# Kernel tuning notes

Measured on AMD Instinct MI355X. Metric: run time of the kernel, lower is better.

## Reference

```python
import jax, jax.numpy as jnp
import numpy as np

ALPHA = 0.2  # LeakyReLU negative slope
NEG_INF = -9e15


def setup_inputs() -> dict:
    key = jax.random.key(0)
    k1, k2, k3, k4 = jax.random.split(key, 4)
    B, N, F_in, F_out = 8, 2048, 256, 128
    h = jax.random.normal(k1, (B, N, F_in), dtype=jnp.float32)
    adj = jax.random.randint(k2, (B, N, N), 0, 2, dtype=jnp.int32)
    # xavier_uniform with gain=1.414
    def xavier(k, shape, gain=1.414):
        fan_in, fan_out = shape[0], shape[1]
        limit = gain * np.sqrt(6.0 / (fan_in + fan_out))
        return jax.random.uniform(k, shape, jnp.float32, -limit, limit)
    W = xavier(k3, (F_in, F_out))
    a = xavier(k4, (2 * F_out, 1))
    return {"h": h, "adj": adj, "W": W, "a": a}


def reference(h, adj, W, a):
    # h: [B,N,F_in], adj: [B,N,N], W: [F_in,F_out], a: [2*F_out,1]
    Wh = jnp.einsum('bnf,fe->bne', h, W)  # [B,N,E]
    E = Wh.shape[-1]
    a_src, a_dst = a[:E, 0], a[E:, 0]
    # e[b,i,j] = leakyrelu(Wh[b,i].a_src + Wh[b,j].a_dst)  (additive decomposition
    # of a @ concat(Wh_i, Wh_j) -- same math, no [B,N,N,2E] intermediate)
    s_src = Wh @ a_src  # [B,N]
    s_dst = Wh @ a_dst  # [B,N]
    e = jax.nn.leaky_relu(s_src[:, :, None] + s_dst[:, None, :], negative_slope=ALPHA)
    e = jnp.where(adj > 0, e, NEG_INF)
    attention = jax.nn.softmax(e, axis=2)  # [B,N,N]
    # dropout p=0.0 / eval mode -> identity
    h_prime = jnp.einsum('bij,bje->bie', attention, Wh)
    return jax.nn.elu(h_prime)  # concat=True
```

## Files before the change

### kernel.cpp

```cpp
#include <hip/hip_runtime.h>
#include <hip/hip_bf16.h>

#define GAT_ALPHA 0.2f
#define LOG2E 1.4426950408889634f

typedef float f32x4 __attribute__((ext_vector_type(4)));
typedef int   i32x4 __attribute__((ext_vector_type(4)));
typedef short bf16x8 __attribute__((ext_vector_type(8)));

static constexpr int Nn  = 2048;
static constexpr int FIN = 256;
static constexpr int FO  = 128;

static __device__ __forceinline__ unsigned short f2bf(float x) {
    __hip_bfloat16 h = __float2bfloat16(x);
    return __builtin_bit_cast(unsigned short, h);
}
static __device__ __forceinline__ float bf2f(unsigned short u) {
    unsigned int v = ((unsigned int)u) << 16;
    return __builtin_bit_cast(float, v);
}

__global__ __launch_bounds__(256) void gat_prep(
        const float* __restrict__ W, const float* __restrict__ a,
        float* __restrict__ wa, unsigned int* __restrict__ md_key)
{
    __shared__ float pr[32][8];
    __shared__ float pd[32][8];
    const int t = threadIdx.x;
    const int kl = t >> 3, seg = t & 7;
    const int k = blockIdx.x * 32 + kl;
    float ps = 0.f, pv = 0.f;
    const float* wr = W + (size_t)k * FO + seg * 16;
    #pragma unroll
    for (int f = 0; f < 16; f += 4) {
        f32x4 wv = *(const f32x4*)(wr + f);
        f32x4 as = *(const f32x4*)(a + seg * 16 + f);
        f32x4 ad = *(const f32x4*)(a + FO + seg * 16 + f);
        ps += wv[0]*as[0] + wv[1]*as[1] + wv[2]*as[2] + wv[3]*as[3];
        pv += wv[0]*ad[0] + wv[1]*ad[1] + wv[2]*ad[2] + wv[3]*ad[3];
    }
    pr[kl][seg] = ps; pd[kl][seg] = pv;
    __syncthreads();
    if (t < 32) {
        float s = 0.f, d = 0.f;
        #pragma unroll
        for (int j = 0; j < 8; ++j) { s += pr[t][j]; d += pd[t][j]; }
        wa[blockIdx.x * 32 + t]       = s;
        wa[256 + blockIdx.x * 32 + t] = d;
    }
    if (blockIdx.x == 0 && t < 8) md_key[t] = 0u;
}

__global__ __launch_bounds__(256) void gat_wh(
        const float* __restrict__ h, const float* __restrict__ W,
        const float* __restrict__ wa, unsigned short* __restrict__ Wp,
        float* __restrict__ s_src, float* __restrict__ s_dst,
        unsigned int* __restrict__ md_key)
{
    __shared__ unsigned short WT[FO][264];
    __shared__ float wal[512];
    __shared__ float sred[64][4][2];
    __shared__ float red64[64];
    const int t  = threadIdx.x;
    const int b  = blockIdx.x & 7;
    const int n0 = (blockIdx.x >> 3) << 6;

    if (t < 128) *(f32x4*)&wal[t * 4] = *(const f32x4*)&wa[t * 4];
    #pragma unroll
    for (int c = 0; c < 32; ++c) {
        int flat = c * 1024 + t * 4;
        int k = flat >> 7, f = flat & 127;
        f32x4 wv = *(const f32x4*)&W[flat];
        WT[f + 0][k] = f2bf(wv[0]);
        WT[f + 1][k] = f2bf(wv[1]);
        WT[f + 2][k] = f2bf(wv[2]);
        WT[f + 3][k] = f2bf(wv[3]);
    }
    __syncthreads();

    {
        const int row = t >> 2, seg = t & 3;
        const float* hp  = h + ((size_t)(b * Nn + n0 + row)) * FIN + seg * 64;
        const float* was = &wal[seg * 64];
        const float* wad = &wal[256 + seg * 64];
        float ps = 0.f, pv = 0.f;
        #pragma unroll
        for (int j = 0; j < 64; j += 4) {
            f32x4 hv = *(const f32x4*)(hp + j);
            f32x4 sv = *(const f32x4*)(was + j);
            f32x4 dv = *(const f32x4*)(wad + j);
            ps += hv[0]*sv[0] + hv[1]*sv[1] + hv[2]*sv[2] + hv[3]*sv[3];
            pv += hv[0]*dv[0] + hv[1]*dv[1] + hv[2]*dv[2] + hv[3]*dv[3];
        }
        sred[row][seg][0] = ps;
        sred[row][seg][1] = pv;
    }
    __syncthreads();
    if (t < 64) {
        float s = sred[t][0][0] + sred[t][1][0] + sred[t][2][0] + sred[t][3][0];
        float d = sred[t][0][1] + sred[t][1][1] + sred[t][2][1] + sred[t][3][1];
        s_src[b * Nn + n0 + t] = s;
        s_dst[b * Nn + n0 + t] = d;
        red64[t] = d;
    }
    __syncthreads();
    if (t < 16) red64[t] = fmaxf(fmaxf(red64[t], red64[t + 16]),
                                 fmaxf(red64[t + 32], red64[t + 48]));
    __syncthreads();
    if (t == 0) {
        float m = red64[0];
        #pragma unroll
        for (int j = 1; j < 16; ++j) m = fmaxf(m, red64[j]);
        unsigned int bits = __builtin_bit_cast(unsigned int, m);
        unsigned int key  = (bits & 0x80000000u) ? ~bits : (bits | 0x80000000u);
        atomicMax(md_key + b, key);
    }

    const int w = t >> 6, lane = t & 63, n16 = lane & 15, quad = lane >> 4;
    const float* ha = h + ((size_t)(b * Nn + n0 + w * 16 + n16)) * FIN + quad * 8;
    f32x4 acc[8] = {};
    #pragma unroll
    for (int ks = 0; ks < 8; ++ks) {
        f32x4 h0 = *(const f32x4*)(ha + ks * 32);
        f32x4 h1 = *(const f32x4*)(ha + ks * 32 + 4);
        bf16x8 af;
        af[0] = (short)f2bf(h0[0]); af[1] = (short)f2bf(h0[1]);
        af[2] = (short)f2bf(h0[2]); af[3] = (short)f2bf(h0[3]);
        af[4] = (short)f2bf(h1[0]); af[5] = (short)f2bf(h1[1]);
        af[6] = (short)f2bf(h1[2]); af[7] = (short)f2bf(h1[3]);
        #pragma unroll
        for (int nt = 0; nt < 8; ++nt) {
            bf16x8 bfr = *(const bf16x8*)&WT[nt * 16 + n16][ks * 32 + quad * 8];
            acc[nt] = __builtin_amdgcn_mfma_f32_16x16x32_bf16(af, bfr, acc[nt], 0, 0, 0);
        }
    }
    {
        const int v      = (n0 >> 5) + (w >> 1);
        const int quad_p = ((w & 1) << 1) + (quad >> 1);
        const int eoff   = (quad & 1) << 2;
        #pragma unroll
        for (int nt = 0; nt < 8; ++nt) {
            ushort4 pk;
            pk.x = f2bf(acc[nt][0]); pk.y = f2bf(acc[nt][1]);
            pk.z = f2bf(acc[nt][2]); pk.w = f2bf(acc[nt][3]);
            size_t idx = ((((size_t)(b << 6) + v) * 8 + nt) * 64 + quad_p * 16 + n16) * 8 + eoff;
            *(ushort4*)&Wp[idx] = pk;
        }
    }
}

__global__ __launch_bounds__(512, 2) void gat_attn(
        const int* __restrict__ adj, const unsigned short* __restrict__ Wp,
        const float* __restrict__ s_src, const float* __restrict__ s_dst,
        const unsigned int* __restrict__ md_key, float* __restrict__ out)
{
    constexpr int AS = 132;
    constexpr int MS = 68;
    __shared__ __align__(16) float smem_f[2 * 64 * AS];
    __shared__ __align__(16) unsigned int mlds[64 * MS];
    __shared__ __align__(16) float dlds[Nn];
    __shared__ float l_red[64];
    unsigned short* ldsw = (unsigned short*)smem_f;

    const int t = threadIdx.x, w = t >> 6, lane = t & 63;
    const int n16 = lane & 15, quad = lane >> 4;
    const int rg = w & 1, jwin = w >> 1;
    const int b  = blockIdx.x & 7;
    const int i0 = (blockIdx.x >> 3) << 6;

    if (t < 64) l_red[t] = 0.f;

    const int* abase = adj + ((size_t)(b * Nn + i0 + w * 8)) * Nn + lane;
    const unsigned short* wsrc = Wp + ((size_t)b << 18);

    int av[16];
    #pragma unroll
    for (int k = 0; k < 16; ++k)
        av[k] = abase[(size_t)(k >> 1) * Nn + ((k & 1) << 6)];
    f32x4 pg[4];
    #pragma unroll
    for (int p = 0; p < 4; ++p)
        pg[p] = *(const f32x4*)(wsrc + p * 4096 + t * 8);
    *(f32x4*)&dlds[t * 4] = *(const f32x4*)(s_dst + b * Nn + t * 4);

    const unsigned int key = md_key[b];
    const unsigned int mb_ = (key & 0x80000000u) ? (key ^ 0x80000000u) : ~key;
    const float mdb = __builtin_bit_cast(float, mb_);
    const int r0 = i0 + rg * 32 + n16;
    const float ssr0 = s_src[b * Nn + r0];
    const float ssr1 = s_src[b * Nn + r0 + 16];
    const float tm0 = ssr0 + mdb, tm1 = ssr1 + mdb;
    const float mi0 = fmaxf(tm0, GAT_ALPHA * tm0) * LOG2E;
    const float mi1 = fmaxf(tm1, GAT_ALPHA * tm1) * LOG2E;
    const float sL0 = ssr0 * LOG2E, sL1 = ssr1 * LOG2E;
    const int jw = (jwin << 5) + (quad << 3);
    const int mrow0 = (rg * 32 + n16) * MS;
    const int mrow1 = mrow0 + 16 * MS;

    #pragma unroll
    for (int k = 0; k < 16; ++k) {
        unsigned long long m = __ballot(av[k] > 0);
        const int rr = k >> 1, c = k & 1;
        if (lane == 0) mlds[(w * 8 + rr) * MS + (c << 1)]     = (unsigned int)m;
        if (lane == 1) mlds[(w * 8 + rr) * MS + (c << 1) + 1] = (unsigned int)(m >> 32);
    }
    #pragma unroll
    for (int p = 0; p < 4; ++p)
        *(f32x4*)&ldsw[p * 4096 + t * 8] = pg[p];

    f32x4 acc[2][8] = {};
    float ls0 = 0.f, ls1 = 0.f;
    __syncthreads();

    for (int s = 0; s < 16; ++s) {
        const int cur = s & 1, nxt = cur ^ 1;
        const int j0 = s << 7;
        if (s < 15) {
            const int coff = (s + 1) << 7;
            #pragma unroll
            for (int k = 0; k < 16; ++k)
                av[k] = abase[(size_t)(k >> 1) * Nn + coff + ((k & 1) << 6)];
        }
        f32x4 g[4];
        if (s < 15) {
            const unsigned short* src = wsrc + (size_t)(s + 1) * 16384;
            #pragma unroll
            for (int p = 0; p < 4; ++p)
                g[p] = *(const f32x4*)(src + p * 4096 + t * 8);
        }
        const unsigned int mw0 = mlds[mrow0 + (s << 2) + jwin];
        const unsigned int mw1 = mlds[mrow1 + (s << 2) + jwin];
        const unsigned int mb0 = (mw0 >> (quad << 3)) & 0xffu;
        const unsigned int mb1 = (mw1 >> (quad << 3)) & 0xffu;
        f32x4 d0 = *(const f32x4*)&dlds[j0 + jw];
        f32x4 d1 = *(const f32x4*)&dlds[j0 + jw + 4];

        bf16x8 af0, af1;
        #pragma unroll
        for (int j = 0; j < 4; ++j) {
            {   float u  = __builtin_fmaf(d0[j], LOG2E, sL0);
                float lr = fmaxf(u, GAT_ALPHA * u);
                float e  = __builtin_amdgcn_exp2f(lr - mi0);
                e = ((mb0 >> j) & 1u) ? e : 0.f;
                unsigned short us = f2bf(e);
                ls0 += bf2f(us); af0[j] = (short)us; }
            {   float u  = __builtin_fmaf(d1[j], LOG2E, sL0);
                float lr = fmaxf(u, GAT_ALPHA * u);
                float e  = __builtin_amdgcn_exp2f(lr - mi0);
                e = ((mb0 >> (4 + j)) & 1u) ? e : 0.f;
                unsigned short us = f2bf(e);
                ls0 += bf2f(us); af0[4 + j] = (short)us; }
            {   float u  = __builtin_fmaf(d0[j], LOG2E, sL1);
                float lr = fmaxf(u, GAT_ALPHA * u);
                float e  = __builtin_amdgcn_exp2f(lr - mi1);
                e = ((mb1 >> j) & 1u) ? e : 0.f;
                unsigned short us = f2bf(e);
                ls1 += bf2f(us); af1[j] = (short)us; }
            {   float u  = __builtin_fmaf(d1[j], LOG2E, sL1);
                float lr = fmaxf(u, GAT_ALPHA * u);
                float e  = __builtin_amdgcn_exp2f(lr - mi1);
                e = ((mb1 >> (4 + j)) & 1u) ? e : 0.f;
                unsigned short us = f2bf(e);
                ls1 += bf2f(us); af1[4 + j] = (short)us; }
        }

        const unsigned short* bbase = &ldsw[cur * 16384 + (jwin << 12) + (lane << 3)];
        #pragma unroll
        for (int nt = 0; nt < 8; ++nt) {
            bf16x8 bfr = *(const bf16x8*)(bbase + (nt << 9));
            acc[0][nt] = __builtin_amdgcn_mfma_f32_16x16x32_bf16(af0, bfr, acc[0][nt], 0, 0, 0);
            acc[1][nt] = __builtin_amdgcn_mfma_f32_16x16x32_bf16(af1, bfr, acc[1][nt], 0, 0, 0);
        }

        if (s < 15) {
            #pragma unroll
            for (int k = 0; k < 16; ++k) {
                unsigned long long m = __ballot(av[k] > 0);
                const int rr = k >> 1, c = k & 1;
                const int wd = ((s + 1) << 2) + (c << 1);
                if (lane == 0) mlds[(w * 8 + rr) * MS + wd]     = (unsigned int)m;
                if (lane == 1) mlds[(w * 8 + rr) * MS + wd + 1] = (unsigned int)(m >> 32);
            }
            #pragma unroll
            for (int p = 0; p < 4; ++p)
                *(f32x4*)&ldsw[nxt * 16384 + p * 4096 + t * 8] = g[p];
        }
        __syncthreads();
    }

    ls0 += __shfl_xor(ls0, 16); ls0 += __shfl_xor(ls0, 32);
    ls1 += __shfl_xor(ls1, 16); ls1 += __shfl_xor(ls1, 32);
    if (quad == 0) {
        atomicAdd(&l_red[rg * 32 + n16], ls0);
        atomicAdd(&l_red[rg * 32 + 16 + n16], ls1);
    }

    float* slot = smem_f + (size_t)(jwin & 1) * (64 * AS);
    const int rbase = rg * 32;
    if (jwin < 2) {
        #pragma unroll
        for (int ig = 0; ig < 2; ++ig)
            #pragma unroll
            for (int nt = 0; nt < 8; ++nt)
                #pragma unroll
                for (int rr = 0; rr < 4; ++rr)
                    slot[(size_t)(rbase + ig * 16 + quad * 4 + rr) * AS + nt * 16 + n16] = acc[ig][nt][rr];
    }
    __syncthreads();
    if (jwin >= 2) {
        #pragma unroll
        for (int ig = 0; ig < 2; ++ig)
            #pragma unroll
            for (int nt = 0; nt < 8; ++nt)
                #pragma unroll
                for (int rr = 0; rr < 4; ++rr)
                    slot[(size_t)(rbase + ig * 16 + quad * 4 + rr) * AS + nt * 16 + n16] += acc[ig][nt][rr];
    }
    __syncthreads();

    float* ob = out + ((size_t)(b * Nn + i0)) * FO;
    #pragma unroll
    for (int c = 0; c < 4; ++c) {
        int flat = c * 2048 + t * 4;
        int m = flat >> 7, f = flat & 127;
        f32x4 v0 = *(const f32x4*)&smem_f[(size_t)m * AS + f];
        f32x4 v1 = *(const f32x4*)&smem_f[(size_t)(64 + m) * AS + f];
        float l = l_red[m];
        f32x4 o;
        #pragma unroll
        for (int j = 0; j < 4; ++j) {
            float x = (v0[j] + v1[j]) / l;
            o[j] = x > 0.f ? x : expm1f(x);
        }
        *(f32x4*)&ob[(size_t)m * FO + f] = o;
    }
}

extern "C" void kernel_launch(void* const* d_in, const int* in_sizes, int n_in,
                              void* d_out, int out_size, void* d_ws, size_t ws_size,
                              hipStream_t stream)
{
    const float* h   = (const float*)d_in[0];
    const int*   adj = (const int*)d_in[1];
    const float* W   = (const float*)d_in[2];
    const float* a   = (const float*)d_in[3];
    float* out = (float*)d_out;

    char* ws = (char*)d_ws;
    unsigned short* Wp  = (unsigned short*)ws;
    float* s_src        = (float*)(ws + 4194304);
    float* s_dst        = (float*)(ws + 4259840);
    float* wa           = (float*)(ws + 4325376);
    unsigned int* md_key= (unsigned int*)(ws + 4327424);

    hipLaunchKernelGGL(gat_prep, dim3(8),   dim3(256), 0, stream, W, a, wa, md_key);
    hipLaunchKernelGGL(gat_wh,   dim3(256), dim3(256), 0, stream, h, W, wa, Wp, s_src, s_dst, md_key);
    hipLaunchKernelGGL(gat_attn, dim3(256), dim3(512), 0, stream, adj, Wp, s_src, s_dst, md_key, out);
}
```

Before: 236.2 us.

## Warp-specialize attention kernel into producer and consumer waves with LDS ring

Splits gat_attn into 8 consumer waves doing exp/MFMA and 4 producer waves that load adjacency masks and packed Wh tiles into a 3-slot LDS ring. Producers and consumers synchronize through LDS flag counters with spin-sleep instead of a block-wide barrier each stage. The aim is to overlap global loads with compute and to drop the per-step __syncthreads. In exchange, occupancy falls from two 512-thread blocks per CU to one 768-thread block, and the spin-waits carry a guard counter that could silently proceed if it expires.

```diff
diff --git a/kernel.cpp b/kernel.cpp
--- a/kernel.cpp
+++ b/kernel.cpp
@@ -150,190 +150,209 @@
     }
 }
 
-__global__ __launch_bounds__(512, 2) void gat_attn(
+__global__ __launch_bounds__(768, 1) void gat_attn(
         const int* __restrict__ adj, const unsigned short* __restrict__ Wp,
         const float* __restrict__ s_src, const float* __restrict__ s_dst,
         const unsigned int* __restrict__ md_key, float* __restrict__ out)
 {
     constexpr int AS = 132;
-    constexpr int MS = 68;
-    __shared__ __align__(16) float smem_f[2 * 64 * AS];
-    __shared__ __align__(16) unsigned int mlds[64 * MS];
+    constexpr int MR = 320;
+    __shared__ __align__(16) float smem_f[24576];
+    __shared__ __align__(16) unsigned int mring[3 * MR];
     __shared__ __align__(16) float dlds[Nn];
     __shared__ float l_red[64];
+    __shared__ unsigned int prod_flag[3], cons_flag[3];
     unsigned short* ldsw = (unsigned short*)smem_f;
 
     const int t = threadIdx.x, w = t >> 6, lane = t & 63;
     const int n16 = lane & 15, quad = lane >> 4;
-    const int rg = w & 1, jwin = w >> 1;
     const int b  = blockIdx.x & 7;
     const int i0 = (blockIdx.x >> 3) << 6;
 
+    if (t < 3) { prod_flag[t] = 0u; cons_flag[t] = 0u; }
     if (t < 64) l_red[t] = 0.f;
-
-    const int* abase = adj + ((size_t)(b * Nn + i0 + w * 8)) * Nn + lane;
+    if (t < 512) *(f32x4*)&dlds[t * 4] = *(const f32x4*)(s_dst + b * Nn + t * 4);
+
     const unsigned short* wsrc = Wp + ((size_t)b << 18);
-
-    int av[16];
-    #pragma unroll
-    for (int k = 0; k < 16; ++k)
-        av[k] = abase[(size_t)(k >> 1) * Nn + ((k & 1) << 6)];
-    f32x4 pg[4];
-    #pragma unroll
-    for (int p = 0; p < 4; ++p)
-        pg[p] = *(const f32x4*)(wsrc + p * 4096 + t * 8);
-    *(f32x4*)&dlds[t * 4] = *(const f32x4*)(s_dst + b * Nn + t * 4);
-
-    const unsigned int key = md_key[b];
-    const unsigned int mb_ = (key & 0x80000000u) ? (key ^ 0x80000000u) : ~key;
-    const float mdb = __builtin_bit_cast(float, mb_);
-    const int r0 = i0 + rg * 32 + n16;
-    const float ssr0 = s_src[b * Nn + r0];
-    const float ssr1 = s_src[b * Nn + r0 + 16];
-    const float tm0 = ssr0 + mdb, tm1 = ssr1 + mdb;
-    const float mi0 = fmaxf(tm0, GAT_ALPHA * tm0) * LOG2E;
-    const float mi1 = fmaxf(tm1, GAT_ALPHA * tm1) * LOG2E;
-    const float sL0 = ssr0 * LOG2E, sL1 = ssr1 * LOG2E;
-    const int jw = (jwin << 5) + (quad << 3);
-    const int mrow0 = (rg * 32 + n16) * MS;
-    const int mrow1 = mrow0 + 16 * MS;
-
-    #pragma unroll
-    for (int k = 0; k < 16; ++k) {
-        unsigned long long m = __ballot(av[k] > 0);
-        const int rr = k >> 1, c = k & 1;
-        if (lane == 0) mlds[(w * 8 + rr) * MS + (c << 1)]     = (unsigned int)m;
-        if (lane == 1) mlds[(w * 8 + rr) * MS + (c << 1) + 1] = (unsigned int)(m >> 32);
-    }
-    #pragma unroll
-    for (int p = 0; p < 4; ++p)
-        *(f32x4*)&ldsw[p * 4096 + t * 8] = pg[p];
+    __syncthreads();
 
     f32x4 acc[2][8] = {};
     float ls0 = 0.f, ls1 = 0.f;
-    __syncthreads();
-
-    for (int s = 0; s < 16; ++s) {
-        const int cur = s & 1, nxt = cur ^ 1;
-        const int j0 = s << 7;
-        if (s < 15) {
-            const int coff = (s + 1) << 7;
-            #pragma unroll
-            for (int k = 0; k < 16; ++k)
-                av[k] = abase[(size_t)(k >> 1) * Nn + coff + ((k & 1) << 6)];
-        }
-        f32x4 g[4];
-        if (s < 15) {
-            const unsigned short* src = wsrc + (size_t)(s + 1) * 16384;
-            #pragma unroll
-            for (int p = 0; p < 4; ++p)
-                g[p] = *(const f32x4*)(src + p * 4096 + t * 8);
-        }
-        const unsigned int mw0 = mlds[mrow0 + (s << 2) + jwin];
-        const unsigned int mw1 = mlds[mrow1 + (s << 2) + jwin];
-        const unsigned int mb0 = (mw0 >> (quad << 3)) & 0xffu;
-        const unsigned int mb1 = (mw1 >> (quad << 3)) & 0xffu;
-        f32x4 d0 = *(const f32x4*)&dlds[j0 + jw];
-        f32x4 d1 = *(const f32x4*)&dlds[j0 + jw + 4];
-
-        bf16x8 af0, af1;
-        #pragma unroll
-        for (int j = 0; j < 4; ++j) {
-            {   float u  = __builtin_fmaf(d0[j], LOG2E, sL0);
-                float lr = fmaxf(u, GAT_ALPHA * u);
-                float e  = __builtin_amdgcn_exp2f(lr - mi0);
-                e = ((mb0 >> j) & 1u) ? e : 0.f;
-                unsigned short us = f2bf(e);
-                ls0 += bf2f(us); af0[j] = (short)us; }
-            {   float u  = __builtin_fmaf(d1[j], LOG2E, sL0);
-                float lr = fmaxf(u, GAT_ALPHA * u);
-                float e  = __builtin_amdgcn_exp2f(lr - mi0);
-                e = ((mb0 >> (4 + j)) & 1u) ? e : 0.f;
-                unsigned short us = f2bf(e);
-                ls0 += bf2f(us); af0[4 + j] = (short)us; }
-            {   float u  = __builtin_fmaf(d0[j], LOG2E, sL1);
-                float lr = fmaxf(u, GAT_ALPHA * u);
-                float e  = __builtin_amdgcn_exp2f(lr - mi1);
-                e = ((mb1 >> j) & 1u) ? e : 0.f;
-                unsigned short us = f2bf(e);
-                ls1 += bf2f(us); af1[j] = (short)us; }
-            {   float u  = __builtin_fmaf(d1[j], LOG2E, sL1);
-                float lr = fmaxf(u, GAT_ALPHA * u);
-                float e  = __builtin_amdgcn_exp2f(lr - mi1);
-                e = ((mb1 >> (4 + j)) & 1u) ? e : 0.f;
-                unsigned short us = f2bf(e);
-                ls1 += bf2f(us); af1[4 + j] = (short)us; }
-        }
-
-        const unsigned short* bbase = &ldsw[cur * 16384 + (jwin << 12) + (lane << 3)];
-        #pragma unroll
-        for (int nt = 0; nt < 8; ++nt) {
-            bf16x8 bfr = *(const bf16x8*)(bbase + (nt << 9));
-            acc[0][nt] = __builtin_amdgcn_mfma_f32_16x16x32_bf16(af0, bfr, acc[0][nt], 0, 0, 0);
-            acc[1][nt] = __builtin_amdgcn_mfma_f32_16x16x32_bf16(af1, bfr, acc[1][nt], 0, 0, 0);
-        }
-
-        if (s < 15) {
-            #pragma unroll
-            for (int k = 0; k < 16; ++k) {
-                unsigned long long m = __ballot(av[k] > 0);
-                const int rr = k >> 1, c = k & 1;
-                const int wd = ((s + 1) << 2) + (c << 1);
-                if (lane == 0) mlds[(w * 8 + rr) * MS + wd]     = (unsigned int)m;
-                if (lane == 1) mlds[(w * 8 + rr) * MS + wd + 1] = (unsigned int)(m >> 32);
-            }
-            #pragma unroll
-            for (int p = 0; p < 4; ++p)
-                *(f32x4*)&ldsw[nxt * 16384 + p * 4096 + t * 8] = g[p];
-        }
-        __syncthreads();
-    }
-
-    ls0 += __shfl_xor(ls0, 16); ls0 += __shfl_xor(ls0, 32);
-    ls1 += __shfl_xor(ls1, 16); ls1 += __shfl_xor(ls1, 32);
-    if (quad == 0) {
-        atomicAdd(&l_red[rg * 32 + n16], ls0);
-        atomicAdd(&l_red[rg * 32 + 16 + n16], ls1);
-    }
-
-    float* slot = smem_f + (size_t)(jwin & 1) * (64 * AS);
-    const int rbase = rg * 32;
-    if (jwin < 2) {
+    const int rg = w & 1, jwin = w >> 1;
+
+    if (w < 8) {
+        const unsigned int key = md_key[b];
+        const unsigned int mb_ = (key & 0x80000000u) ? (key ^ 0x80000000u) : ~key;
+        const float mdb = __builtin_bit_cast(float, mb_);
+        const int r0 = i0 + rg * 32 + n16;
+        const float ssr0 = s_src[b * Nn + r0];
+        const float ssr1 = s_src[b * Nn + r0 + 16];
+        const float tm0 = ssr0 + mdb, tm1 = ssr1 + mdb;
+        const float mi0 = fmaxf(tm0, GAT_ALPHA * tm0) * LOG2E;
+        const float mi1 = fmaxf(tm1, GAT_ALPHA * tm1) * LOG2E;
+        const float sL0 = ssr0 * LOG2E, sL1 = ssr1 * LOG2E;
+        const int jw = (jwin << 5) + (quad << 3);
+        const int mr0 = (rg * 32 + n16) * 5 + jwin;
+        const int mr1 = mr0 + 16 * 5;
+
+        for (int s = 0; s < 16; ++s) {
+            const int slot = s % 3;
+            const unsigned int ptarget = 4u * (unsigned int)(s / 3 + 1);
+            {
+                volatile unsigned int* pf = &prod_flag[slot];
+                int guard = 0;
+                while (*pf < ptarget && guard < (1 << 26)) {
+                    ++guard; __builtin_amdgcn_s_sleep(2);
+                }
+            }
+            const int j0 = s << 7;
+            const unsigned int mw0 = mring[slot * MR + mr0];
+            const unsigned int mw1 = mring[slot * MR + mr1];
+            const unsigned int mb0 = (mw0 >> (quad << 3)) & 0xffu;
+            const unsigned int mb1 = (mw1 >> (quad << 3)) & 0xffu;
+            f32x4 d0 = *(const f32x4*)&dlds[j0 + jw];
+            f32x4 d1 = *(const f32x4*)&dlds[j0 + jw + 4];
+
+            bf16x8 af0, af1;
+            #pragma unroll
+            for (int j = 0; j < 4; ++j) {
+                {   float u  = __builtin_fmaf(d0[j], LOG2E, sL0);
+                    float lr = fmaxf(u, GAT_ALPHA * u);
+                    float e  = __builtin_amdgcn_exp2f(lr - mi0);
+                    e = ((mb0 >> j) & 1u) ? e : 0.f;
+                    unsigned short us = f2bf(e);
+                    ls0 += bf2f(us); af0[j] = (short)us; }
+                {   float u  = __builtin_fmaf(d1[j], LOG2E, sL0);
+                    float lr = fmaxf(u, GAT_ALPHA * u);
+                    float e  = __builtin_amdgcn_exp2f(lr - mi0);
+                    e = ((mb0 >> (4 + j)) & 1u) ? e : 0.f;
+                    unsigned short us = f2bf(e);
+                    ls0 += bf2f(us); af0[4 + j] = (short)us; }
+                {   float u  = __builtin_fmaf(d0[j], LOG2E, sL1);
+                    float lr = fmaxf(u, GAT_ALPHA * u);
+                    float e  = __builtin_amdgcn_exp2f(lr - mi1);
+                    e = ((mb1 >> j) & 1u) ? e : 0.f;
+                    unsigned short us = f2bf(e);
+                    ls1 += bf2f(us); af1[j] = (short)us; }
+                {   float u  = __builtin_fmaf(d1[j], LOG2E, sL1);
+                    float lr = fmaxf(u, GAT_ALPHA * u);
+                    float e  = __builtin_amdgcn_exp2f(lr - mi1);
+                    e = ((mb1 >> (4 + j)) & 1u) ? e : 0.f;
+                    unsigned short us = f2bf(e);
+                    ls1 += bf2f(us); af1[4 + j] = (short)us; }
+            }
+
+            const unsigned short* bbase = &ldsw[slot * 16384 + (jwin << 12) + (lane << 3)];
+            #pragma unroll
+            for (int nt = 0; nt < 8; ++nt) {
+                bf16x8 bfr = *(const bf16x8*)(bbase + (nt << 9));
+                acc[0][nt] = __builtin_amdgcn_mfma_f32_16x16x32_bf16(af0, bfr, acc[0][nt], 0, 0, 0);
+                acc[1][nt] = __builtin_amdgcn_mfma_f32_16x16x32_bf16(af1, bfr, acc[1][nt], 0, 0, 0);
+            }
+            if (lane == 0) atomicAdd(&cons_flag[slot], 1u);
+        }
+    } else {
+        const int p = w - 8;
+        const int pl = (p << 6) + lane;
+        const int* arow0 = adj + ((size_t)(b * Nn + i0 + (p << 4))) * Nn + lane;
+
+        for (int s = 0; s < 16; ++s) {
+            const int slot = s % 3;
+            const int r = s / 3;
+            if (r > 0) {
+                const unsigned int ctarget = 8u * (unsigned int)r;
+                volatile unsigned int* cf = &cons_flag[slot];
+                int guard = 0;
+                while (*cf < ctarget && guard < (1 << 26)) {
+                    ++guard; __builtin_amdgcn_s_sleep(2);
+                }
+            }
+            const int j0 = s << 7;
+            const unsigned short* src = wsrc + (size_t)s * 16384;
+            f32x4 g[8];
+            #pragma unroll
+            for (int q = 0; q < 8; ++q)
+                g[q] = *(const f32x4*)(src + q * 2048 + pl * 8);
+            int av[32];
+            #pragma unroll
+            for (int rr = 0; rr < 16; ++rr) {
+                av[2 * rr]     = arow0[(size_t)rr * Nn + j0];
+                av[2 * rr + 1] = arow0[(size_t)rr * Nn + j0 + 64];
+            }
+            #pragma unroll
+            for (int rr = 0; rr < 16; ++rr) {
+                unsigned long long m0 = __ballot(av[2 * rr]     > 0);
+                unsigned long long m1 = __ballot(av[2 * rr + 1] > 0);
+                const int mbx = slot * MR + ((p << 4) + rr) * 5;
+                if (lane == 0) {
+                    mring[mbx + 0] = (unsigned int)m0;
+                    mring[mbx + 2] = (unsigned int)m1;
+                }
+                if (lane == 1) {
+                    mring[mbx + 1] = (unsigned int)(m0 >> 32);
+                    mring[mbx + 3] = (unsigned int)(m1 >> 32);
+                }
+            }
+            #pragma unroll
+            for (int q = 0; q < 8; ++q)
+                *(f32x4*)&ldsw[slot * 16384 + q * 2048 + pl * 8] = g[q];
+            asm volatile("s_waitcnt lgkmcnt(0)" ::: "memory");
+            if (lane == 0) atomicAdd(&prod_flag[slot], 1u);
+        }
+    }
+
+    __syncthreads();
+
+    if (w < 8) {
+        ls0 += __shfl_xor(ls0, 16); ls0 += __shfl_xor(ls0, 32);
+        ls1 += __shfl_xor(ls1, 16); ls1 += __shfl_xor(ls1, 32);
+        if (quad == 0) {
+            atomicAdd(&l_red[rg * 32 + n16], ls0);
+            atomicAdd(&l_red[rg * 32 + 16 + n16], ls1);
+        }
+        if (jwin < 2) {
+            float* slotp = smem_f + (size_t)(jwin & 1) * (64 * AS);
+            const int rbase = rg * 32;
+            #pragma unroll
+            for (int ig = 0; ig < 2; ++ig)
+                #pragma unroll
+                for (int nt = 0; nt < 8; ++nt)
+                    #pragma unroll
+                    for (int rr = 0; rr < 4; ++rr)
+                        slotp[(size_t)(rbase + ig * 16 + quad * 4 + rr) * AS + nt * 16 + n16] = acc[ig][nt][rr];
+        }
+    }
+    __syncthreads();
+    if (w < 8 && jwin >= 2) {
+        float* slotp = smem_f + (size_t)(jwin & 1) * (64 * AS);
+        const int rbase = rg * 32;
         #pragma unroll
         for (int ig = 0; ig < 2; ++ig)
             #pragma unroll
             for (int nt = 0; nt < 8; ++nt)
                 #pragma unroll
                 for (int rr = 0; rr < 4; ++rr)
-                    slot[(size_t)(rbase + ig * 16 + quad * 4 + rr) * AS + nt * 16 + n16] = acc[ig][nt][rr];
-    }
-    __syncthreads();
-    if (jwin >= 2) {
-        #pragma unroll
-        for (int ig = 0; ig < 2; ++ig)
-            #pragma unroll
-            for (int nt = 0; nt < 8; ++nt)
-                #pragma unroll
-                for (int rr = 0; rr < 4; ++rr)
-                    slot[(size_t)(rbase + ig * 16 + quad * 4 + rr) * AS + nt * 16 + n16] += acc[ig][nt][rr];
-    }
-    __syncthreads();
-
-    float* ob = out + ((size_t)(b * Nn + i0)) * FO;
-    #pragma unroll
-    for (int c = 0; c < 4; ++c) {
-        int flat = c * 2048 + t * 4;
-        int m = flat >> 7, f = flat & 127;
-        f32x4 v0 = *(const f32x4*)&smem_f[(size_t)m * AS + f];
-        f32x4 v1 = *(const f32x4*)&smem_f[(size_t)(64 + m) * AS + f];
-        float l = l_red[m];
-        f32x4 o;
-        #pragma unroll
-        for (int j = 0; j < 4; ++j) {
-            float x = (v0[j] + v1[j]) / l;
-            o[j] = x > 0.f ? x : expm1f(x);
-        }
-        *(f32x4*)&ob[(size_t)m * FO + f] = o;
+                    slotp[(size_t)(rbase + ig * 16 + quad * 4 + rr) * AS + nt * 16 + n16] += acc[ig][nt][rr];
+    }
+    __syncthreads();
+
+    if (t < 512) {
+        float* ob = out + ((size_t)(b * Nn + i0)) * FO;
+        #pragma unroll
+        for (int c = 0; c < 4; ++c) {
+            int flat = c * 2048 + t * 4;
+            int m = flat >> 7, f = flat & 127;
+            f32x4 v0 = *(const f32x4*)&smem_f[(size_t)m * AS + f];
+            f32x4 v1 = *(const f32x4*)&smem_f[(size_t)(64 + m) * AS + f];
+            float l = l_red[m];
+            f32x4 o;
+            #pragma unroll
+            for (int j = 0; j < 4; ++j) {
+                float x = (v0[j] + v1[j]) / l;
+                o[j] = x > 0.f ? x : expm1f(x);
+            }
+            *(f32x4*)&ob[(size_t)m * FO + f] = o;
+        }
     }
 }
 
@@ -356,5 +375,5 @@
 
     hipLaunchKernelGGL(gat_prep, dim3(8),   dim3(256), 0, stream, W, a, wa, md_key);
     hipLaunchKernelGGL(gat_wh,   dim3(256), dim3(256), 0, stream, h, W, wa, Wp, s_src, s_dst, md_key);
-    hipLaunchKernelGGL(gat_attn, dim3(256), dim3(512), 0, stream, adj, Wp, s_src, s_dst, md_key, out);
-}
+    hipLaunchKernelGGL(gat_attn, dim3(256), dim3(768), 0, stream, adj, Wp, s_src, s_dst, md_key, out);
+}
```

Result: no change. 234.0 us (-0.9%).
